# Optimization experiments

Hardware: AMD Instinct MI355X
Metric: run time of the kernel (lower is better)

## Reference

```python
import jax, jax.numpy as jnp
import numpy as np

H = 32     # hidden_size
S = 64     # sequence length (steps)


def positional_encoding(seq_len, d_model):
    # faithful to source: position * div_term with div_term = 10000**(arange/ d)
    position = jnp.arange(seq_len, dtype=jnp.float32)[:, None]
    div_term = 10000.0 ** (jnp.arange(0, d_model, 2, dtype=jnp.float32) / d_model)
    ang = position * div_term                      # [S, H/2]
    pe = jnp.zeros((seq_len, d_model), dtype=jnp.float32)
    pe = pe.at[:, 0::2].set(jnp.sin(ang))
    pe = pe.at[:, 1::2].set(jnp.cos(ang))
    return pe                                      # [seq_len, H]


def setup_inputs() -> dict:
    key = jax.random.key(0)
    ks = jax.random.split(key, 6)
    B, K, NP, V = 32, 64, 100000, 4096
    return {
        "neighbor_ids": jax.random.randint(ks[0], (B, S, K, 2), 0, V, dtype=jnp.int32),
        "param_indices": jax.random.randint(ks[1], (B, S, K), 0, NP, dtype=jnp.int32),
        "weights": jax.random.uniform(ks[2], (NP, H, H), minval=-0.5, maxval=0.5, dtype=jnp.float32),
        "biases": jax.random.uniform(ks[3], (NP, H), minval=-0.5, maxval=0.5, dtype=jnp.float32),
        "node_bias": jax.random.uniform(ks[4], (V, H), minval=-0.5, maxval=0.5, dtype=jnp.float32),
        "positions": jnp.ones((512,), dtype=jnp.float32),
    }


def reference(neighbor_ids, param_indices, weights, biases, node_bias, positions):
    B = neighbor_ids.shape[0]
    gelu = lambda x: jax.nn.gelu(x, approximate=False)  # torch nn.GELU default (erf)
    pe = positional_encoding(512, H)                    # [512, H]

    # initial energy: ones/H + node_bias[src of first edge] + pe[0]
    init_energy = gelu(1.0 / H + node_bias[neighbor_ids[:, 0, 0, 0]] + pe[0])  # [B, H]

    pos_logits = positions[:S]        # [S]
    steps = jnp.arange(S)

    def step(carry, i):
        cache, loss_sum = carry       # cache: [B, S, H] (rows >= i are zero)
        # softmax pooling over the growing cache (positions[:i])
        mask = steps < i
        w = jax.nn.softmax(jnp.where(mask, pos_logits, -1e30))  # [S]
        pooled = jnp.einsum('s,bsh->bh', w, cache)              # [B, H]
        energy = jnp.where(i == 0, init_energy, pooled)         # [B, H]

        idx = jax.lax.dynamic_index_in_dim(param_indices, i, axis=1, keepdims=False)  # [B, K]
        Wm = weights[idx]            # [B, K, H, H] per-edge weight gather
        bm = biases[idx]             # [B, K, H]
        nxt = gelu(jnp.einsum('bh,bkhd->bkd', energy, Wm) + bm + pe[i + 1])  # [B, K, H]

        enorm = jnp.linalg.norm(nxt, axis=-1)                   # [B, K]
        # CrossEntropy with label 0
        loss_i = jnp.mean(jax.nn.logsumexp(enorm, axis=1) - enorm[:, 0])
        cache = cache.at[:, i, :].set(nxt[:, 0])                # append gold-edge output
        return (cache, loss_sum + loss_i), None

    cache0 = jnp.zeros((B, S, H), dtype=jnp.float32)
    (_, loss_sum), _ = jax.lax.scan(step, (cache0, jnp.float32(0.0)), steps)
    return loss_sum / S
```

## Files before the change

kernel.cpp:

```cpp
#include <hip/hip_runtime.h>
#include <math.h>

#define H 32
#define S 64
#define K 64
#define B 32
#define NTILE 2048
#define NBIGW 4064
#define SENTU 0x7fc00042u

__device__ __forceinline__ float gelu_f(float x) {
    return 0.5f * x * (1.0f + erff(x * 0.70710678118654752440f));
}

__device__ __forceinline__ void lds_fence() {
    asm volatile("s_waitcnt lgkmcnt(0)" ::: "memory");
}

__device__ __forceinline__ float bcast_lane(float v, int lane) {
    return __uint_as_float(__builtin_amdgcn_readlane(__float_as_uint(v), lane));
}


__global__ void precompute_kernel(float* __restrict__ pe, float* __restrict__ energies) {
    int t = blockIdx.x * 256 + threadIdx.x;
    if (t < B * S * H) energies[t] = __uint_as_float(SENTU);
    if (t < 65 * 32) {
        int p = t >> 5, c = t & 31;
        int iq = c >> 1;
        double dt = pow(10000.0, (double)(2 * iq) / 32.0);
        float ang = (float)p * (float)dt;
        double v = (c & 1) ? cos((double)ang) : sin((double)ang);
        pe[t] = (float)v;
    }
}

__global__ __launch_bounds__(256, 4) void fused_kernel(
    const int* __restrict__ neighbor_ids,
    const int* __restrict__ param_indices,
    const float* __restrict__ weights,
    const float* __restrict__ biases,
    const float* __restrict__ node_bias,
    const float* __restrict__ pe_g,
    const float* __restrict__ positions,
    float* energies,
    float* __restrict__ ennorm) {
    const int bid = blockIdx.x;
    const int tid = threadIdx.x;
    const int wv = tid >> 6;
    const int lane = tid & 63;

    __shared__ int c_idx[S];
    __shared__ float c_pos[S];
    __shared__ float c_pe[(S + 1) * H];
    __shared__ float c_bias[S * H];

    if (bid < 32 && wv == 0) {
        __builtin_amdgcn_s_setprio(3);
        const int b = bid;
        const int l = lane;
        const int r = l >> 5;
        const int d = l & 31;

        c_idx[l] = param_indices[((size_t)(b * S + l)) * K];
        c_pos[l] = positions[l];
        for (int t = l; t < (S + 1) * H; t += 64) c_pe[t] = pe_g[t];
        lds_fence();

        for (int t = l; t < S * H; t += 64)
            c_bias[t] = biases[(size_t)c_idx[t >> 5] * H + (t & 31)];

        float w0[16], w1[16], w2[16], w3[16];
        const int rowoff = r * 16;
        auto loadW = [&](float (&wb)[16], int step) {
            const float* Wp = weights + (size_t)c_idx[step] * (H * H) + (size_t)rowoff * H + d;
            #pragma unroll
            for (int j = 0; j < 16; ++j) wb[j] = Wp[j * H];
        };
        loadW(w0, 0); loadW(w1, 1); loadW(w2, 2); loadW(w3, 3);

        float init_e;
        {
            int nid = neighbor_ids[(size_t)b * S * K * 2];
            init_e = gelu_f(0.03125f + node_bias[(size_t)nid * H + d] + c_pe[d]);
        }
        lds_fence();

        float m = -1e30f, ssum = 0.0f, A = 0.0f, nxtprev = 0.0f;

        auto step = [&](float (&wb)[16], int i) {
            float e;
            if (i == 0) {
                e = init_e;
            } else {
                float p = c_pos[i - 1];
                if (p > m) { float sc = expf(m - p); A *= sc; ssum *= sc; m = p; }
                float wgt = expf(p - m);
                A = fmaf(wgt, nxtprev, A);
                ssum += wgt;
                e = A / ssum;
            }
            if (r == 0)
                __hip_atomic_store(&energies[((size_t)(b * S + i)) * H + d], e,
                                   __ATOMIC_RELAXED, __HIP_MEMORY_SCOPE_AGENT);

            float acc = 0.0f;
            #pragma unroll
            for (int j = 0; j < 16; ++j) {
                float e0 = bcast_lane(e, j);
                float e1 = bcast_lane(e, 16 + j);
                acc = fmaf(r ? e1 : e0, wb[j], acc);
            }
            acc += __shfl_xor(acc, 32, 64);
            nxtprev = gelu_f(acc + c_bias[i * H + d] + c_pe[(i + 1) * H + d]);
            if (i + 4 < S) loadW(wb, i + 4);
        };

        #pragma unroll
        for (int ii = 0; ii < S; ii += 4) {
            step(w0, ii); step(w1, ii + 1); step(w2, ii + 2); step(w3, ii + 3);
        }
    } else {
        const int count = (bid < 32) ? (bid + 1) : 32;
        const int rank = bid * 4 + wv - count;
        const int rowq = lane >> 4;
        const int dp = lane & 15;

        for (int s = rank; s < 4 * NTILE; s += NBIGW) {
            const int i = s >> 7;
            const int b = (s >> 2) & 31;
            const int quarter = s & 3;
            const int bi = b * S + i;

            float ereg[8];
            for (;;) {
                #pragma unroll
                for (int hh = 0; hh < 8; ++hh)
                    ereg[hh] = __hip_atomic_load(&energies[(size_t)bi * H + hh * 4 + rowq],
                                                 __ATOMIC_RELAXED, __HIP_MEMORY_SCOPE_AGENT);
                int bad = 0;
                #pragma unroll
                for (int hh = 0; hh < 8; ++hh) bad |= (ereg[hh] != ereg[hh]);
                if (!__any(bad)) break;
                __builtin_amdgcn_s_sleep(10);
            }

            float pex = pe_g[(i + 1) * H + 2 * dp];
            float pey = pe_g[(i + 1) * H + 2 * dp + 1];
            int idxv = 0;
            if (lane < 16) idxv = param_indices[(size_t)bi * K + quarter * 16 + lane];

            int ia = __builtin_amdgcn_readlane(idxv, 0);
            int ib = __builtin_amdgcn_readlane(idxv, 8);
            float2 ca[8], cb[8], bca, bcb;
            {
                const float2* Wa = (const float2*)(weights + (size_t)ia * (H * H));
                const float2* Wb = (const float2*)(weights + (size_t)ib * (H * H));
                #pragma unroll
                for (int hh = 0; hh < 8; ++hh) {
                    ca[hh] = Wa[(hh * 4 + rowq) * 16 + dp];
                    cb[hh] = Wb[(hh * 4 + rowq) * 16 + dp];
                }
                bca = *(const float2*)(biases + (size_t)ia * H + 2 * dp);
                bcb = *(const float2*)(biases + (size_t)ib * H + 2 * dp);
            }

            float norm = 0.0f;
            #pragma unroll
            for (int it = 0; it < 8; ++it) {
                float2 na[8], nb[8], bna, bnb;
                if (it < 7) {
                    int ja = __builtin_amdgcn_readlane(idxv, it + 1);
                    int jb = __builtin_amdgcn_readlane(idxv, it + 9);
                    const float2* Wa = (const float2*)(weights + (size_t)ja * (H * H));
                    const float2* Wb = (const float2*)(weights + (size_t)jb * (H * H));
                    #pragma unroll
                    for (int hh = 0; hh < 8; ++hh) {
                        na[hh] = Wa[(hh * 4 + rowq) * 16 + dp];
                        nb[hh] = Wb[(hh * 4 + rowq) * 16 + dp];
                    }
                    bna = *(const float2*)(biases + (size_t)ja * H + 2 * dp);
                    bnb = *(const float2*)(biases + (size_t)jb * H + 2 * dp);
                }

                float axa = 0, aya = 0, axb = 0, ayb = 0;
                #pragma unroll
                for (int hh = 0; hh < 8; ++hh) {
                    axa = fmaf(ereg[hh], ca[hh].x, axa);
                    aya = fmaf(ereg[hh], ca[hh].y, aya);
                    axb = fmaf(ereg[hh], cb[hh].x, axb);
                    ayb = fmaf(ereg[hh], cb[hh].y, ayb);
                }
                axa += __shfl_xor(axa, 16, 64); aya += __shfl_xor(aya, 16, 64);
                axb += __shfl_xor(axb, 16, 64); ayb += __shfl_xor(ayb, 16, 64);
                axa += __shfl_xor(axa, 32, 64); aya += __shfl_xor(aya, 32, 64);
                axb += __shfl_xor(axb, 32, 64); ayb += __shfl_xor(ayb, 32, 64);
                float v0a = gelu_f(axa + bca.x + pex);
                float v1a = gelu_f(aya + bca.y + pey);
                float v0b = gelu_f(axb + bcb.x + pex);
                float v1b = gelu_f(ayb + bcb.y + pey);
                float ssa = fmaf(v0a, v0a, v1a * v1a);
                float ssb = fmaf(v0b, v0b, v1b * v1b);
                #pragma unroll
                for (int mk = 8; mk; mk >>= 1) {
                    ssa += __shfl_xor(ssa, mk, 64);
                    ssb += __shfl_xor(ssb, mk, 64);
                }
                norm = (lane == it)     ? ssa : norm;
                norm = (lane == it + 8) ? ssb : norm;

                if (it < 7) {
                    #pragma unroll
                    for (int hh = 0; hh < 8; ++hh) { ca[hh] = na[hh]; cb[hh] = nb[hh]; }
                    bca = bna; bcb = bnb;
                }
            }
            if (lane < 16)
                ennorm[(size_t)bi * K + quarter * 16 + lane] = sqrtf(norm);
        }
    }
}

__global__ __launch_bounds__(256) void reduce1_kernel(const float* __restrict__ ennorm,
                                                      float* __restrict__ partials) {
    int bid = blockIdx.x;
    int tid = threadIdx.x;
    int wv = tid >> 6;
    int lane = tid & 63;
    __shared__ float sh[4];

    float wsum = 0.0f;
    for (int j = 0; j < 16; ++j) {
        int t = bid * 64 + wv * 16 + j;
        float en = ennorm[(size_t)t * K + lane];
        float mm = en;
        #pragma unroll
        for (int mk = 32; mk; mk >>= 1) mm = fmaxf(mm, __shfl_xor(mm, mk, 64));
        float sx = expf(en - mm);
        #pragma unroll
        for (int mk = 32; mk; mk >>= 1) sx += __shfl_xor(sx, mk, 64);
        float en0 = bcast_lane(en, 0);
        wsum += mm + logf(sx) - en0;
    }
    if (lane == 0) sh[wv] = wsum;
    __syncthreads();
    if (tid == 0) partials[bid] = (sh[0] + sh[1]) + (sh[2] + sh[3]);
}

__global__ void reduce2_kernel(const float* __restrict__ partials, float* __restrict__ out) {
    if (threadIdx.x == 0) {
        float s = 0.0f;
        for (int j = 0; j < 32; ++j) s += partials[j];
        out[0] = s * (1.0f / 2048.0f);
    }
}

extern "C" void kernel_launch(void* const* d_in, const int* in_sizes, int n_in,
                              void* d_out, int out_size, void* d_ws, size_t ws_size,
                              hipStream_t stream) {
    const int*   neighbor_ids  = (const int*)d_in[0];
    const int*   param_indices = (const int*)d_in[1];
    const float* weights       = (const float*)d_in[2];
    const float* biases        = (const float*)d_in[3];
    const float* node_bias     = (const float*)d_in[4];
    const float* positions     = (const float*)d_in[5];

    float* ws       = (float*)d_ws;
    float* pe       = ws;
    float* energies = ws + 2080;
    float* ennorm   = ws + 67616;
    float* partials = ws + 198688;

    hipLaunchKernelGGL(precompute_kernel, dim3(256), dim3(256), 0, stream,
                       pe, energies);
    hipLaunchKernelGGL(fused_kernel, dim3(1024), dim3(256), 0, stream,
                       neighbor_ids, param_indices, weights, biases, node_bias,
                       pe, positions, energies, ennorm);
    hipLaunchKernelGGL(reduce1_kernel, dim3(32), dim3(256), 0, stream,
                       ennorm, partials);
    hipLaunchKernelGGL(reduce2_kernel, dim3(1), dim3(64), 0, stream,
                       partials, (float*)d_out);
}
```

Measured before the change: 111.9 us.

## Fuse logsumexp and final reduction into main kernel via atomic completion counters

Removes the two trailing reduction kernels. Each (batch, step) tile counts its four quarter-wave completions with an atomic counter, and the last finisher computes that tile's logsumexp loss term. A global done-counter then lets the last tile sum all terms and write the output. This saves two kernel launches and their serialization gaps, at the cost of atomics, vmcnt drains and relaxed-ordering memory visibility that could be fragile.

Result: slower. 114.4 us (+2.2%).

```diff
diff --git a/kernel.cpp b/kernel.cpp
--- a/kernel.cpp
+++ b/kernel.cpp
@@ -17,14 +17,21 @@
     asm volatile("s_waitcnt lgkmcnt(0)" ::: "memory");
 }
 
+__device__ __forceinline__ void vm_drain() {
+    asm volatile("s_waitcnt vmcnt(0)" ::: "memory");
+}
+
 __device__ __forceinline__ float bcast_lane(float v, int lane) {
     return __uint_as_float(__builtin_amdgcn_readlane(__float_as_uint(v), lane));
 }
 
 
-__global__ void precompute_kernel(float* __restrict__ pe, float* __restrict__ energies) {
+__global__ void precompute_kernel(float* __restrict__ pe, float* __restrict__ energies,
+                                  int* __restrict__ tile_ctr, int* __restrict__ done_ctr) {
     int t = blockIdx.x * 256 + threadIdx.x;
     if (t < B * S * H) energies[t] = __uint_as_float(SENTU);
+    if (t < NTILE) tile_ctr[t] = 0;
+    if (t == NTILE) done_ctr[0] = 0;
     if (t < 65 * 32) {
         int p = t >> 5, c = t & 31;
         int iq = c >> 1;
@@ -44,7 +51,11 @@
     const float* __restrict__ pe_g,
     const float* __restrict__ positions,
     float* energies,
-    float* __restrict__ ennorm) {
+    float* ennorm,
+    float* lse,
+    int* tile_ctr,
+    int* done_ctr,
+    float* __restrict__ out) {
     const int bid = blockIdx.x;
     const int tid = threadIdx.x;
     const int wv = tid >> 6;
@@ -216,42 +227,48 @@
                 }
             }
             if (lane < 16)
-                ennorm[(size_t)bi * K + quarter * 16 + lane] = sqrtf(norm);
+                __hip_atomic_store(&ennorm[(size_t)bi * K + quarter * 16 + lane],
+                                   sqrtf(norm), __ATOMIC_RELAXED, __HIP_MEMORY_SCOPE_AGENT);
+            vm_drain();
+
+            int old = 0;
+            if (lane == 0)
+                old = __hip_atomic_fetch_add(&tile_ctr[bi], 1,
+                                             __ATOMIC_RELAXED, __HIP_MEMORY_SCOPE_AGENT);
+            old = __shfl(old, 0, 64);
+
+            if (old == 3) {
+                float en = __hip_atomic_load(&ennorm[(size_t)bi * K + lane],
+                                             __ATOMIC_RELAXED, __HIP_MEMORY_SCOPE_AGENT);
+                float mm = en;
+                #pragma unroll
+                for (int mk = 32; mk; mk >>= 1) mm = fmaxf(mm, __shfl_xor(mm, mk, 64));
+                float sx = expf(en - mm);
+                #pragma unroll
+                for (int mk = 32; mk; mk >>= 1) sx += __shfl_xor(sx, mk, 64);
+                float en0 = bcast_lane(en, 0);
+                if (lane == 0)
+                    __hip_atomic_store(&lse[bi], mm + logf(sx) - en0,
+                                       __ATOMIC_RELAXED, __HIP_MEMORY_SCOPE_AGENT);
+                vm_drain();
+
+                int old2 = 0;
+                if (lane == 0)
+                    old2 = __hip_atomic_fetch_add(done_ctr, 1,
+                                                  __ATOMIC_RELAXED, __HIP_MEMORY_SCOPE_AGENT);
+                old2 = __shfl(old2, 0, 64);
+
+                if (old2 == NTILE - 1) {
+                    float fsum = 0.0f;
+                    for (int j = 0; j < 32; ++j)
+                        fsum += __hip_atomic_load(&lse[lane + 64 * j],
+                                                  __ATOMIC_RELAXED, __HIP_MEMORY_SCOPE_AGENT);
+                    #pragma unroll
+                    for (int mk = 32; mk; mk >>= 1) fsum += __shfl_xor(fsum, mk, 64);
+                    if (lane == 0) out[0] = fsum * (1.0f / 2048.0f);
+                }
+            }
         }
-    }
-}
-
-__global__ __launch_bounds__(256) void reduce1_kernel(const float* __restrict__ ennorm,
-                                                      float* __restrict__ partials) {
-    int bid = blockIdx.x;
-    int tid = threadIdx.x;
-    int wv = tid >> 6;
-    int lane = tid & 63;
-    __shared__ float sh[4];
-
-    float wsum = 0.0f;
-    for (int j = 0; j < 16; ++j) {
-        int t = bid * 64 + wv * 16 + j;
-        float en = ennorm[(size_t)t * K + lane];
-        float mm = en;
-        #pragma unroll
-        for (int mk = 32; mk; mk >>= 1) mm = fmaxf(mm, __shfl_xor(mm, mk, 64));
-        float sx = expf(en - mm);
-        #pragma unroll
-        for (int mk = 32; mk; mk >>= 1) sx += __shfl_xor(sx, mk, 64);
-        float en0 = bcast_lane(en, 0);
-        wsum += mm + logf(sx) - en0;
-    }
-    if (lane == 0) sh[wv] = wsum;
-    __syncthreads();
-    if (tid == 0) partials[bid] = (sh[0] + sh[1]) + (sh[2] + sh[3]);
-}
-
-__global__ void reduce2_kernel(const float* __restrict__ partials, float* __restrict__ out) {
-    if (threadIdx.x == 0) {
-        float s = 0.0f;
-        for (int j = 0; j < 32; ++j) s += partials[j];
-        out[0] = s * (1.0f / 2048.0f);
     }
 }
 
@@ -269,15 +286,14 @@
     float* pe       = ws;
     float* energies = ws + 2080;
     float* ennorm   = ws + 67616;
-    float* partials = ws + 198688;
+    float* lse      = ws + 198688;
+    int*   tile_ctr = (int*)(ws + 200736);
+    int*   done_ctr = (int*)(ws + 202784);
 
     hipLaunchKernelGGL(precompute_kernel, dim3(256), dim3(256), 0, stream,
-                       pe, energies);
+                       pe, energies, tile_ctr, done_ctr);
     hipLaunchKernelGGL(fused_kernel, dim3(1024), dim3(256), 0, stream,
                        neighbor_ids, param_indices, weights, biases, node_bias,
-                       pe, positions, energies, ennorm);
-    hipLaunchKernelGGL(reduce1_kernel, dim3(32), dim3(256), 0, stream,
-                       ennorm, partials);
-    hipLaunchKernelGGL(reduce2_kernel, dim3(1), dim3(64), 0, stream,
-                       partials, (float*)d_out);
-}
+                       pe, positions, energies, ennorm, lse, tile_ctr, done_ctr,
+                       (float*)d_out);
+}
```
